# Optimization experiments

Measured on AMD Instinct MI355X. Metric: run time of the kernel, lower is better.

The kernel has to match this reference:

```python
import jax, jax.numpy as jnp
import numpy as np

B, S, D, H, HID, NUM_POS = 8, 512, 512, 8, 2048, 1
DIM = D // H
EPS = 1e-3  # keras LayerNormalization default epsilon


def _ln(x, g, b):
    mu = jnp.mean(x, axis=-1, keepdims=True)
    var = jnp.mean(jnp.square(x - mu), axis=-1, keepdims=True)
    return (x - mu) * jax.lax.rsqrt(var + EPS) * g + b


def setup_inputs() -> dict:
    key = jax.random.key(0)
    ks = jax.random.split(key, 12)
    s = 0.02
    return {
        "values": jax.random.normal(ks[0], (B, S, D), jnp.float32),
        "values_mask": jnp.ones((B, S), jnp.bool_),
        "ln0_g": jnp.ones((D,), jnp.float32),
        "ln0_b": jnp.zeros((D,), jnp.float32),
        "W0a": jax.random.normal(ks[1], (D, HID), jnp.float32) * s,
        "b0a": jnp.zeros((HID,), jnp.float32),
        "W0b": jax.random.normal(ks[2], (HID, 3 * D), jnp.float32) * s,
        "b0b": jnp.zeros((3 * D,), jnp.float32),
        "Wp": jax.random.normal(ks[3], (2 * NUM_POS + 1, D), jnp.float32) * s,
        "bp": jnp.zeros((D,), jnp.float32),
        "ln1_g": jnp.ones((D,), jnp.float32),
        "ln1_b": jnp.zeros((D,), jnp.float32),
        "W1a": jax.random.normal(ks[4], (D, HID), jnp.float32) * s,
        "b1a": jnp.zeros((HID,), jnp.float32),
        "W1b": jax.random.normal(ks[5], (HID, D), jnp.float32) * s,
        "b1b": jnp.zeros((D,), jnp.float32),
    }


def reference(values, values_mask, ln0_g, ln0_b, W0a, b0a, W0b, b0b,
              Wp, bp, ln1_g, ln1_b, W1a, b1a, W1b, b1b):
    # Block0: LN -> Dense(HID, relu) -> Dense(3D)  (QKV projection)
    h = _ln(values, ln0_g, ln0_b)
    x = jax.nn.relu(h @ W0a + b0a) @ W0b + b0b            # [B,S,3D]
    x = x.reshape(B, S, H, 3 * DIM).transpose(0, 2, 1, 3)  # [B,H,S,3*dim]
    q, k, v = x[..., :DIM], x[..., DIM:2 * DIM], x[..., 2 * DIM:]

    # relative positions (l2r identity permutation): one-hot(clip(j-i)) @ Wp + bp
    idx = jnp.clip(jnp.arange(S)[None, :] - jnp.arange(S)[:, None],
                   -NUM_POS, NUM_POS) + NUM_POS            # [S,S] in {0,1,2}
    pos = Wp[idx] + bp                                     # [S,S,D]
    pos = pos.reshape(S, S, H, DIM).transpose(2, 0, 1, 3)  # [H,S,S,dim]

    # bias_{bhqk} = q_{bhqd} . pos_{hqkd}
    bias = jnp.einsum('bhqd,hqkd->bhqk', q, pos)

    scores = bias + jnp.einsum('bhqd,bhkd->bhqk', q, k) / jnp.sqrt(
        jnp.asarray(DIM, jnp.float32))

    mask = values_mask[:, None, :, None] & values_mask[:, None, None, :]
    causal = jnp.tril(jnp.ones((S, S), jnp.bool_))
    mask = mask & causal[None, None]
    att = jax.nn.softmax(jnp.where(mask, scores, -999999.0), axis=-1)

    o = jnp.einsum('bhqk,bhkd->bhqd', att, v)              # [B,H,S,dim]
    o = o.transpose(0, 2, 1, 3).reshape(B, S, D)
    values = values + o

    # Block1 FFN residual
    h = _ln(values, ln1_g, ln1_b)
    values = values + (jax.nn.relu(h @ W1a + b1a) @ W1b + b1b)
    return values
```

## Files before the change

kernel.cpp:

```cpp
#include <hip/hip_runtime.h>
#include <hip/hip_bf16.h>
#include <stdint.h>

using hbf = __hip_bfloat16;
typedef __bf16 bf16x8 __attribute__((ext_vector_type(8)));
typedef float f32x4 __attribute__((ext_vector_type(4)));

#define MFMA16(a, b, c) __builtin_amdgcn_mfma_f32_16x16x32_bf16((a), (b), (c), 0, 0, 0)

__device__ __forceinline__ void async_copy16(const void* gsrc, void* ldst) {
  __builtin_amdgcn_global_load_lds((const __attribute__((address_space(1))) void*)gsrc,
                                   (__attribute__((address_space(3))) void*)ldst,
                                   16, 0, 0);
}

__global__ __launch_bounds__(256) void wtrans_kernel(const float* __restrict__ W,
                                                     hbf* __restrict__ Wt,
                                                     int K, int N) {
  __shared__ float tile[64][65];
  const int n0 = blockIdx.x * 64, k0 = blockIdx.y * 64;
  const int tid = threadIdx.x;
#pragma unroll
  for (int i = 0; i < 16; ++i) {
    int idx = tid + i * 256;
    int r = idx >> 6, c = idx & 63;
    tile[r][c] = W[(size_t)(k0 + r) * N + n0 + c];
  }
  __syncthreads();
#pragma unroll
  for (int i = 0; i < 16; ++i) {
    int idx = tid + i * 256;
    int r = idx >> 6, c = idx & 63;
    Wt[(size_t)(n0 + r) * K + k0 + c] = __float2bfloat16(tile[c][r]);
  }
}

__global__ __launch_bounds__(256) void ln0_kernel(const float* __restrict__ x,
                                                  const float* __restrict__ g,
                                                  const float* __restrict__ bt,
                                                  hbf* __restrict__ h) {
  const int row = blockIdx.x * 4 + (threadIdx.x >> 6);
  const int l = threadIdx.x & 63;
  const float* xr = x + (size_t)row * 512;
  float v[8], s = 0.f, s2 = 0.f;
#pragma unroll
  for (int i = 0; i < 8; ++i) {
    float t = xr[l + 64 * i];
    v[i] = t; s += t; s2 += t * t;
  }
#pragma unroll
  for (int off = 32; off; off >>= 1) { s += __shfl_xor(s, off); s2 += __shfl_xor(s2, off); }
  float mu = s * (1.f / 512.f);
  float rs = rsqrtf(s2 * (1.f / 512.f) - mu * mu + 1e-3f);
  hbf* hr = h + (size_t)row * 512;
#pragma unroll
  for (int i = 0; i < 8; ++i) {
    int c = l + 64 * i;
    hr[c] = __float2bfloat16((v[i] - mu) * rs * g[c] + bt[c]);
  }
}

__global__ __launch_bounds__(256) void lnadd_kernel(const float* __restrict__ values,
                                                    const float* __restrict__ obuf,
                                                    const float* __restrict__ g,
                                                    const float* __restrict__ bt,
                                                    float* __restrict__ res1,
                                                    hbf* __restrict__ h2) {
  const int row = blockIdx.x * 4 + (threadIdx.x >> 6);
  const int l = threadIdx.x & 63;
  const float* vr = values + (size_t)row * 512;
  const float* orow = obuf + (size_t)row * 512;
  float* rr = res1 + (size_t)row * 512;
  float v[8], s = 0.f, s2 = 0.f;
#pragma unroll
  for (int i = 0; i < 8; ++i) {
    int c = l + 64 * i;
    float t = vr[c] + orow[c];
    v[i] = t; s += t; s2 += t * t;
    rr[c] = t;
  }
#pragma unroll
  for (int off = 32; off; off >>= 1) { s += __shfl_xor(s, off); s2 += __shfl_xor(s2, off); }
  float mu = s * (1.f / 512.f);
  float rs = rsqrtf(s2 * (1.f / 512.f) - mu * mu + 1e-3f);
  hbf* hr = h2 + (size_t)row * 512;
#pragma unroll
  for (int i = 0; i < 8; ++i) {
    int c = l + 64 * i;
    hr[c] = __float2bfloat16((v[i] - mu) * rs * g[c] + bt[c]);
  }
}

template <int EPI>
__global__ __launch_bounds__(256) void gemm_bt(const hbf* __restrict__ A,
                                               const hbf* __restrict__ Bt,
                                               const float* __restrict__ bias,
                                               const float* __restrict__ resid,
                                               void* __restrict__ outp,
                                               int M, int N, int K) {
  __shared__ hbf As[128 * 64];
  __shared__ hbf Bs[64 * 64];
  const int tid = threadIdx.x;
  const int lane = tid & 63;
  const int w = tid >> 6;
  const int wm = w >> 1, wn = w & 1;

  const int nbx = gridDim.x;
  const int nwg = nbx * gridDim.y;
  const int bid = blockIdx.y * nbx + blockIdx.x;
  const int cpx = nwg >> 3;
  const int sw = (bid & 7) * cpx + (bid >> 3);
  const int m0 = (sw / nbx) * 128, n0 = (sw % nbx) * 64;

  f32x4 acc[4][2] = {};

  int ar[4], ac[4];
#pragma unroll
  for (int p = 0; p < 4; ++p) {
    int off = p * 4096 + tid * 16;
    int r = off >> 7, sl = (off >> 4) & 7;
    ar[p] = r;
    ac[p] = sl ^ (r & 7);
  }

  for (int kt = 0; kt < K; kt += 64) {
#pragma unroll
    for (int p = 0; p < 4; ++p)
      async_copy16(A + (size_t)(m0 + ar[p]) * K + kt + ac[p] * 8,
                   (char*)As + p * 4096 + tid * 16);
#pragma unroll
    for (int p = 0; p < 2; ++p)
      async_copy16(Bt + (size_t)(n0 + ar[p]) * K + kt + ac[p] * 8,
                   (char*)Bs + p * 4096 + tid * 16);
    __syncthreads();
    const int cq = lane >> 4, lr = lane & 15;
    bf16x8 af[2][4], bg[2][2];
#pragma unroll
    for (int i = 0; i < 4; ++i) {
      int m = wm * 64 + i * 16 + lr;
#pragma unroll
      for (int kk = 0; kk < 2; ++kk) {
        int sl = (kk * 4 + cq) ^ (m & 7);
        af[kk][i] = *reinterpret_cast<const bf16x8*>((const char*)As + m * 128 + sl * 16);
      }
    }
#pragma unroll
    for (int j = 0; j < 2; ++j) {
      int n = wn * 32 + j * 16 + lr;
#pragma unroll
      for (int kk = 0; kk < 2; ++kk) {
        int sl = (kk * 4 + cq) ^ (n & 7);
        bg[kk][j] = *reinterpret_cast<const bf16x8*>((const char*)Bs + n * 128 + sl * 16);
      }
    }
#pragma unroll
    for (int kk = 0; kk < 2; ++kk)
#pragma unroll
      for (int i = 0; i < 4; ++i)
#pragma unroll
        for (int j = 0; j < 2; ++j)
          acc[i][j] = MFMA16(af[kk][i], bg[kk][j], acc[i][j]);
    __syncthreads();
  }

#pragma unroll
  for (int j = 0; j < 2; ++j) {
    int col = n0 + wn * 32 + j * 16 + (lane & 15);
    float bcol = bias[col];
#pragma unroll
    for (int i = 0; i < 4; ++i) {
      int rowb = m0 + wm * 64 + i * 16 + (lane >> 4) * 4;
#pragma unroll
      for (int r = 0; r < 4; ++r) {
        int row = rowb + r;
        float v = acc[i][j][r] + bcol;
        if (EPI == 0) {
          v = v > 0.f ? v : 0.f;
          ((hbf*)outp)[(size_t)row * N + col] = __float2bfloat16(v);
        } else if (EPI == 1) {
          ((hbf*)outp)[(size_t)row * N + col] = __float2bfloat16(v);
        } else {
          ((float*)outp)[(size_t)row * N + col] = v + resid[(size_t)row * N + col];
        }
      }
    }
  }
}

__global__ __launch_bounds__(256) void vtrans_kernel(const hbf* __restrict__ X2,
                                                     hbf* __restrict__ vT) {
  __shared__ hbf tile[64][80];
  const int bh = blockIdx.x, s0 = blockIdx.y * 64;
  const int b = bh >> 3, h = bh & 7;
  const int tid = threadIdx.x;
#pragma unroll
  for (int i = 0; i < 2; ++i) {
    int chunk = tid + i * 256;
    int r = chunk >> 3, c8 = (chunk & 7) * 8;
    const hbf* src = X2 + (size_t)(b * 512 + s0 + r) * 1536 + h * 192 + 128 + c8;
    *reinterpret_cast<bf16x8*>(&tile[r][c8]) = *reinterpret_cast<const bf16x8*>(src);
  }
  __syncthreads();
#pragma unroll
  for (int i = 0; i < 2; ++i) {
    int chunk = tid + i * 256;
    int d = chunk >> 3, s8 = (chunk & 7) * 8;
    bf16x8 v;
#pragma unroll
    for (int j = 0; j < 8; ++j) v[j] = *reinterpret_cast<const __bf16*>(&tile[s8 + j][d]);
    *reinterpret_cast<bf16x8*>(vT + ((size_t)bh * 64 + d) * 512 + s0 + s8) = v;
  }
}

__global__ __launch_bounds__(256) void posbias_kernel(const hbf* __restrict__ X2,
                                                      const float* __restrict__ Wp,
                                                      const float* __restrict__ bp,
                                                      float* __restrict__ bb) {
  int idx = blockIdx.x * 256 + threadIdx.x;
  int c = idx >> 15;
  int r = idx & 32767;
  int bh = r >> 9, q = r & 511;
  int b = bh >> 3, h = bh & 7;
  const hbf* qp = X2 + (size_t)(b * 512 + q) * 1536 + h * 192;
  const float* wr = Wp + c * 512 + h * 64;
  const float* br = bp + h * 64;
  float s = 0.f;
#pragma unroll
  for (int d8 = 0; d8 < 8; ++d8) {
    bf16x8 qv = *reinterpret_cast<const bf16x8*>(qp + d8 * 8);
#pragma unroll
    for (int j = 0; j < 8; ++j) s += (float)qv[j] * (wr[d8 * 8 + j] + br[d8 * 8 + j]);
  }
  bb[idx] = s;
}

__global__ __launch_bounds__(256) void attn_kernel(const hbf* __restrict__ X2,
                                                   const hbf* __restrict__ vT,
                                                   const float* __restrict__ bb,
                                                   float* __restrict__ obuf) {
  __shared__ hbf p_lds[4][16][32];
  const int bh = blockIdx.x;
  const int b = bh >> 3, h = bh & 7;
  const int q0 = blockIdx.y * 64;
  const int tid = threadIdx.x;
  const int lane = tid & 63, w = tid >> 6;
  const int qbase = q0 + w * 16;

  bf16x8 qa[2];
  {
    int qrow = qbase + (lane & 15);
    const hbf* qp = X2 + (size_t)(b * 512 + qrow) * 1536 + h * 192 + (lane >> 4) * 8;
#pragma unroll
    for (int c = 0; c < 2; ++c) qa[c] = *reinterpret_cast<const bf16x8*>(qp + c * 32);
  }
  float bias0[4], bias1[4];
#pragma unroll
  for (int r = 0; r < 4; ++r) {
    int qr = qbase + (lane >> 4) * 4 + r;
    bias0[r] = bb[bh * 512 + qr];
    bias1[r] = bb[32768 + bh * 512 + qr];
  }

  float mrow[4], lsum[4];
  f32x4 oacc[4];
#pragma unroll
  for (int r = 0; r < 4; ++r) { mrow[r] = -1e30f; lsum[r] = 0.f; }
#pragma unroll
  for (int nt = 0; nt < 4; ++nt) oacc[nt] = (f32x4){0.f, 0.f, 0.f, 0.f};

  const int qhi = qbase + 15;
  const int nchunks = (qhi >> 5) + 1;
  for (int ch = 0; ch < nchunks; ++ch) {
    const int k32 = ch * 32;
    f32x4 z = {0.f, 0.f, 0.f, 0.f};
    f32x4 s0, s1;
    {
      const hbf* kp = X2 + (size_t)(b * 512 + k32 + (lane & 15)) * 1536 + h * 192 + 64 + (lane >> 4) * 8;
      bf16x8 kb = *reinterpret_cast<const bf16x8*>(kp);
      s0 = MFMA16(qa[0], kb, z);
      kb = *reinterpret_cast<const bf16x8*>(kp + 32);
      s0 = MFMA16(qa[1], kb, s0);
      const hbf* kp1 = kp + 16 * 1536;
      kb = *reinterpret_cast<const bf16x8*>(kp1);
      s1 = MFMA16(qa[0], kb, z);
      kb = *reinterpret_cast<const bf16x8*>(kp1 + 32);
      s1 = MFMA16(qa[1], kb, s1);
    }
    const int col0 = k32 + (lane & 15);
    const int col1 = col0 + 16;
    float p0[4], p1[4], alpha[4];
#pragma unroll
    for (int r = 0; r < 4; ++r) {
      int q = qbase + (lane >> 4) * 4 + r;
      float sc0 = (col0 > q) ? -1e30f : (s0[r] * 0.125f + (col0 == q ? bias1[r] : bias0[r]));
      float sc1 = (col1 > q) ? -1e30f : (s1[r] * 0.125f + (col1 == q ? bias1[r] : bias0[r]));
      float cm = fmaxf(sc0, sc1);
#pragma unroll
      for (int off = 1; off < 16; off <<= 1) cm = fmaxf(cm, __shfl_xor(cm, off));
      float mn = fmaxf(mrow[r], cm);
      alpha[r] = __expf(mrow[r] - mn);
      mrow[r] = mn;
      float e0 = __expf(sc0 - mn), e1 = __expf(sc1 - mn);
      p0[r] = e0; p1[r] = e1;
      float ps = e0 + e1;
#pragma unroll
      for (int off = 1; off < 16; off <<= 1) ps += __shfl_xor(ps, off);
      lsum[r] = lsum[r] * alpha[r] + ps;
    }
#pragma unroll
    for (int nt = 0; nt < 4; ++nt)
#pragma unroll
      for (int r = 0; r < 4; ++r) oacc[nt][r] *= alpha[r];
#pragma unroll
    for (int r = 0; r < 4; ++r) {
      p_lds[w][(lane >> 4) * 4 + r][lane & 15] = __float2bfloat16(p0[r]);
      p_lds[w][(lane >> 4) * 4 + r][16 + (lane & 15)] = __float2bfloat16(p1[r]);
    }
    bf16x8 pa = *reinterpret_cast<const bf16x8*>(&p_lds[w][lane & 15][(lane >> 4) * 8]);
#pragma unroll
    for (int nt = 0; nt < 4; ++nt) {
      const hbf* vp = vT + ((size_t)bh * 64 + nt * 16 + (lane & 15)) * 512 + k32 + (lane >> 4) * 8;
      bf16x8 vb = *reinterpret_cast<const bf16x8*>(vp);
      oacc[nt] = MFMA16(pa, vb, oacc[nt]);
    }
  }
#pragma unroll
  for (int r = 0; r < 4; ++r) {
    float rl = 1.f / lsum[r];
    int q = qbase + (lane >> 4) * 4 + r;
    float* orow = obuf + (size_t)(b * 512 + q) * 512 + h * 64;
#pragma unroll
    for (int nt = 0; nt < 4; ++nt) orow[nt * 16 + (lane & 15)] = oacc[nt][r] * rl;
  }
}

extern "C" void kernel_launch(void* const* d_in, const int* in_sizes, int n_in,
                              void* d_out, int out_size, void* d_ws, size_t ws_size,
                              hipStream_t stream) {
  const float* values = (const float*)d_in[0];
  const float* ln0_g = (const float*)d_in[2];
  const float* ln0_b = (const float*)d_in[3];
  const float* W0a = (const float*)d_in[4];
  const float* b0a = (const float*)d_in[5];
  const float* W0b = (const float*)d_in[6];
  const float* b0b = (const float*)d_in[7];
  const float* Wp = (const float*)d_in[8];
  const float* bp = (const float*)d_in[9];
  const float* ln1_g = (const float*)d_in[10];
  const float* ln1_b = (const float*)d_in[11];
  const float* W1a = (const float*)d_in[12];
  const float* b1a = (const float*)d_in[13];
  const float* W1b = (const float*)d_in[14];
  const float* b1b = (const float*)d_in[15];

  char* ws = (char*)d_ws;
  hbf* W0a_t = (hbf*)(ws + (0ull << 20));
  hbf* W0b_t = (hbf*)(ws + (2ull << 20));
  hbf* W1a_t = (hbf*)(ws + (8ull << 20));
  hbf* W1b_t = (hbf*)(ws + (10ull << 20));
  hbf* hbuf = (hbf*)(ws + (12ull << 20));
  hbf* X1 = (hbf*)(ws + (16ull << 20));
  hbf* X2 = (hbf*)(ws + (32ull << 20));
  float* obuf = (float*)(ws + (44ull << 20));
  hbf* vT = (hbf*)(ws + (52ull << 20));
  float* bb = (float*)(ws + (56ull << 20));
  float* res1 = (float*)(ws + (57ull << 20));
  hbf* X3 = X1;
  hbf* h2 = hbuf;

  wtrans_kernel<<<dim3(32, 8), 256, 0, stream>>>(W0a, W0a_t, 512, 2048);
  wtrans_kernel<<<dim3(24, 32), 256, 0, stream>>>(W0b, W0b_t, 2048, 1536);
  wtrans_kernel<<<dim3(32, 8), 256, 0, stream>>>(W1a, W1a_t, 512, 2048);
  wtrans_kernel<<<dim3(8, 32), 256, 0, stream>>>(W1b, W1b_t, 2048, 512);

  ln0_kernel<<<1024, 256, 0, stream>>>(values, ln0_g, ln0_b, hbuf);

  gemm_bt<0><<<dim3(32, 32), 256, 0, stream>>>(hbuf, W0a_t, b0a, nullptr, X1, 4096, 2048, 512);
  gemm_bt<1><<<dim3(24, 32), 256, 0, stream>>>(X1, W0b_t, b0b, nullptr, X2, 4096, 1536, 2048);

  vtrans_kernel<<<dim3(64, 8), 256, 0, stream>>>(X2, vT);
  posbias_kernel<<<384, 256, 0, stream>>>(X2, Wp, bp, bb);
  attn_kernel<<<dim3(64, 8), 256, 0, stream>>>(X2, vT, bb, obuf);

  lnadd_kernel<<<1024, 256, 0, stream>>>(values, obuf, ln1_g, ln1_b, res1, h2);

  gemm_bt<0><<<dim3(32, 32), 256, 0, stream>>>(h2, W1a_t, b1a, nullptr, X3, 4096, 2048, 512);
  gemm_bt<2><<<dim3(8, 32), 256, 0, stream>>>(X3, W1b_t, b1b, res1, (float*)d_out, 4096, 512, 2048);
}
```

Before: 247.2 us.

## Double-buffer GEMM tiles, merge weight transposes, narrow last GEMM tile

The GEMM kernel now double-buffers its LDS tiles, issuing the async copy for the next K tile before computing on the current one, so global loads overlap with MFMA work. It is also templated on the N tile width, and the final FFN GEMM (N=512) uses a 32-wide tile to launch twice as many workgroups. The four weight-transpose launches are merged into a single kernel that dispatches on block index, and the posbias grid shrinks from 384 to 256 blocks. The costs are doubled LDS per block, which may lower occupancy, and a posbias grid change whose correctness depends on how that kernel walks its work.

```diff
diff --git a/kernel.cpp b/kernel.cpp
--- a/kernel.cpp
+++ b/kernel.cpp
@@ -14,23 +14,32 @@
                                    16, 0, 0);
 }
 
-__global__ __launch_bounds__(256) void wtrans_kernel(const float* __restrict__ W,
-                                                     hbf* __restrict__ Wt,
-                                                     int K, int N) {
+__global__ __launch_bounds__(256) void wtrans_all(const float* __restrict__ W0a,
+                                                  const float* __restrict__ W0b,
+                                                  const float* __restrict__ W1a,
+                                                  const float* __restrict__ W1b,
+                                                  hbf* __restrict__ T0a, hbf* __restrict__ T0b,
+                                                  hbf* __restrict__ T1a, hbf* __restrict__ T1b) {
   __shared__ float tile[64][65];
-  const int n0 = blockIdx.x * 64, k0 = blockIdx.y * 64;
+  const int idx = blockIdx.x;
+  const float* W; hbf* Wt; int K, N, nt, i;
+  if (idx < 256)        { W = W0a; Wt = T0a; K = 512;  N = 2048; nt = 32; i = idx; }
+  else if (idx < 1024)  { W = W0b; Wt = T0b; K = 2048; N = 1536; nt = 24; i = idx - 256; }
+  else if (idx < 1280)  { W = W1a; Wt = T1a; K = 512;  N = 2048; nt = 32; i = idx - 1024; }
+  else                  { W = W1b; Wt = T1b; K = 2048; N = 512;  nt = 8;  i = idx - 1280; }
+  const int n0 = (i % nt) * 64, k0 = (i / nt) * 64;
   const int tid = threadIdx.x;
 #pragma unroll
-  for (int i = 0; i < 16; ++i) {
-    int idx = tid + i * 256;
-    int r = idx >> 6, c = idx & 63;
+  for (int t = 0; t < 16; ++t) {
+    int q = tid + t * 256;
+    int r = q >> 6, c = q & 63;
     tile[r][c] = W[(size_t)(k0 + r) * N + n0 + c];
   }
   __syncthreads();
 #pragma unroll
-  for (int i = 0; i < 16; ++i) {
-    int idx = tid + i * 256;
-    int r = idx >> 6, c = idx & 63;
+  for (int t = 0; t < 16; ++t) {
+    int q = tid + t * 256;
+    int r = q >> 6, c = q & 63;
     Wt[(size_t)(n0 + r) * K + k0 + c] = __float2bfloat16(tile[c][r]);
   }
 }
@@ -91,28 +100,33 @@
   }
 }
 
-template <int EPI>
+template <int EPI, int BN>
 __global__ __launch_bounds__(256) void gemm_bt(const hbf* __restrict__ A,
                                                const hbf* __restrict__ Bt,
                                                const float* __restrict__ bias,
                                                const float* __restrict__ resid,
                                                void* __restrict__ outp,
                                                int M, int N, int K) {
-  __shared__ hbf As[128 * 64];
-  __shared__ hbf Bs[64 * 64];
+  constexpr int WCOLS = (BN == 64) ? 2 : 1;
+  constexpr int WROWS = 4 / WCOLS;
+  constexpr int MI = 128 / (WROWS * 16);
+  constexpr int NJ = BN / (WCOLS * 16);
+  constexpr int BCH = BN / 32;
+  __shared__ hbf As[2][128 * 64];
+  __shared__ hbf Bs[2][BN * 64];
   const int tid = threadIdx.x;
   const int lane = tid & 63;
   const int w = tid >> 6;
-  const int wm = w >> 1, wn = w & 1;
+  const int wm = w / WCOLS, wn = w % WCOLS;
 
   const int nbx = gridDim.x;
   const int nwg = nbx * gridDim.y;
   const int bid = blockIdx.y * nbx + blockIdx.x;
   const int cpx = nwg >> 3;
   const int sw = (bid & 7) * cpx + (bid >> 3);
-  const int m0 = (sw / nbx) * 128, n0 = (sw % nbx) * 64;
-
-  f32x4 acc[4][2] = {};
+  const int m0 = (sw / nbx) * 128, n0 = (sw % nbx) * BN;
+
+  f32x4 acc[MI][NJ] = {};
 
   int ar[4], ac[4];
 #pragma unroll
@@ -123,53 +137,61 @@
     ac[p] = sl ^ (r & 7);
   }
 
-  for (int kt = 0; kt < K; kt += 64) {
+  auto stage = [&](int buf, int kt) {
 #pragma unroll
     for (int p = 0; p < 4; ++p)
       async_copy16(A + (size_t)(m0 + ar[p]) * K + kt + ac[p] * 8,
-                   (char*)As + p * 4096 + tid * 16);
-#pragma unroll
-    for (int p = 0; p < 2; ++p)
+                   (char*)As[buf] + p * 4096 + tid * 16);
+#pragma unroll
+    for (int p = 0; p < BCH; ++p)
       async_copy16(Bt + (size_t)(n0 + ar[p]) * K + kt + ac[p] * 8,
-                   (char*)Bs + p * 4096 + tid * 16);
-    __syncthreads();
+                   (char*)Bs[buf] + p * 4096 + tid * 16);
+  };
+
+  stage(0, 0);
+  __syncthreads();
+  int cur = 0;
+
+  for (int kt = 0; kt < K; kt += 64) {
+    if (kt + 64 < K) stage(cur ^ 1, kt + 64);
     const int cq = lane >> 4, lr = lane & 15;
-    bf16x8 af[2][4], bg[2][2];
-#pragma unroll
-    for (int i = 0; i < 4; ++i) {
-      int m = wm * 64 + i * 16 + lr;
+    bf16x8 af[2][MI], bg[2][NJ];
+#pragma unroll
+    for (int i = 0; i < MI; ++i) {
+      int m = wm * (MI * 16) + i * 16 + lr;
 #pragma unroll
       for (int kk = 0; kk < 2; ++kk) {
         int sl = (kk * 4 + cq) ^ (m & 7);
-        af[kk][i] = *reinterpret_cast<const bf16x8*>((const char*)As + m * 128 + sl * 16);
+        af[kk][i] = *reinterpret_cast<const bf16x8*>((const char*)As[cur] + m * 128 + sl * 16);
       }
     }
 #pragma unroll
-    for (int j = 0; j < 2; ++j) {
-      int n = wn * 32 + j * 16 + lr;
+    for (int j = 0; j < NJ; ++j) {
+      int n = wn * (NJ * 16) + j * 16 + lr;
 #pragma unroll
       for (int kk = 0; kk < 2; ++kk) {
         int sl = (kk * 4 + cq) ^ (n & 7);
-        bg[kk][j] = *reinterpret_cast<const bf16x8*>((const char*)Bs + n * 128 + sl * 16);
+        bg[kk][j] = *reinterpret_cast<const bf16x8*>((const char*)Bs[cur] + n * 128 + sl * 16);
       }
     }
 #pragma unroll
     for (int kk = 0; kk < 2; ++kk)
 #pragma unroll
-      for (int i = 0; i < 4; ++i)
-#pragma unroll
-        for (int j = 0; j < 2; ++j)
+      for (int i = 0; i < MI; ++i)
+#pragma unroll
+        for (int j = 0; j < NJ; ++j)
           acc[i][j] = MFMA16(af[kk][i], bg[kk][j], acc[i][j]);
     __syncthreads();
-  }
-
-#pragma unroll
-  for (int j = 0; j < 2; ++j) {
-    int col = n0 + wn * 32 + j * 16 + (lane & 15);
+    cur ^= 1;
+  }
+
+#pragma unroll
+  for (int j = 0; j < NJ; ++j) {
+    int col = n0 + wn * (NJ * 16) + j * 16 + (lane & 15);
     float bcol = bias[col];
 #pragma unroll
-    for (int i = 0; i < 4; ++i) {
-      int rowb = m0 + wm * 64 + i * 16 + (lane >> 4) * 4;
+    for (int i = 0; i < MI; ++i) {
+      int rowb = m0 + wm * (MI * 16) + i * 16 + (lane >> 4) * 4;
 #pragma unroll
       for (int r = 0; r < 4; ++r) {
         int row = rowb + r;
@@ -368,22 +390,19 @@
   hbf* X3 = X1;
   hbf* h2 = hbuf;
 
-  wtrans_kernel<<<dim3(32, 8), 256, 0, stream>>>(W0a, W0a_t, 512, 2048);
-  wtrans_kernel<<<dim3(24, 32), 256, 0, stream>>>(W0b, W0b_t, 2048, 1536);
-  wtrans_kernel<<<dim3(32, 8), 256, 0, stream>>>(W1a, W1a_t, 512, 2048);
-  wtrans_kernel<<<dim3(8, 32), 256, 0, stream>>>(W1b, W1b_t, 2048, 512);
+  wtrans_all<<<1536, 256, 0, stream>>>(W0a, W0b, W1a, W1b, W0a_t, W0b_t, W1a_t, W1b_t);
 
   ln0_kernel<<<1024, 256, 0, stream>>>(values, ln0_g, ln0_b, hbuf);
 
-  gemm_bt<0><<<dim3(32, 32), 256, 0, stream>>>(hbuf, W0a_t, b0a, nullptr, X1, 4096, 2048, 512);
-  gemm_bt<1><<<dim3(24, 32), 256, 0, stream>>>(X1, W0b_t, b0b, nullptr, X2, 4096, 1536, 2048);
+  gemm_bt<0, 64><<<dim3(32, 32), 256, 0, stream>>>(hbuf, W0a_t, b0a, nullptr, X1, 4096, 2048, 512);
+  gemm_bt<1, 64><<<dim3(24, 32), 256, 0, stream>>>(X1, W0b_t, b0b, nullptr, X2, 4096, 1536, 2048);
 
   vtrans_kernel<<<dim3(64, 8), 256, 0, stream>>>(X2, vT);
-  posbias_kernel<<<384, 256, 0, stream>>>(X2, Wp, bp, bb);
+  posbias_kernel<<<256, 256, 0, stream>>>(X2, Wp, bp, bb);
   attn_kernel<<<dim3(64, 8), 256, 0, stream>>>(X2, vT, bb, obuf);
 
   lnadd_kernel<<<1024, 256, 0, stream>>>(values, obuf, ln1_g, ln1_b, res1, h2);
 
-  gemm_bt<0><<<dim3(32, 32), 256, 0, stream>>>(h2, W1a_t, b1a, nullptr, X3, 4096, 2048, 512);
-  gemm_bt<2><<<dim3(8, 32), 256, 0, stream>>>(X3, W1b_t, b1b, res1, (float*)d_out, 4096, 512, 2048);
-}
+  gemm_bt<0, 64><<<dim3(32, 32), 256, 0, stream>>>(h2, W1a_t, b1a, nullptr, X3, 4096, 2048, 512);
+  gemm_bt<2, 32><<<dim3(16, 32), 256, 0, stream>>>(X3, W1b_t, b1b, res1, (float*)d_out, 4096, 512, 2048);
+}
```

Result: faster. 232.3 us (-6.0%).
